# Kernel optimization log

Hardware: AMD Instinct MI355X
Metric: run time of the kernel (lower is better)

## Reference

```python
import jax, jax.numpy as jnp
import numpy as np

ROI = 9
GROUPS = 32

def _gn(x, gamma, beta, eps):
    B, C, H, W = x.shape
    xr = x.reshape(B, GROUPS, C // GROUPS, H, W)
    m = xr.mean(axis=(2, 3, 4), keepdims=True)
    v = xr.var(axis=(2, 3, 4), keepdims=True)
    xr = (xr - m) / jnp.sqrt(v + eps)
    x = xr.reshape(B, C, H, W)
    if gamma is not None:
        x = x * gamma[None, :, None, None] + beta[None, :, None, None]
    return x

def _conv(x, w, b, pad):
    y = jax.lax.conv_general_dilated(x, w, (1, 1), [(pad, pad), (pad, pad)],
                                     dimension_numbers=('NCHW', 'OIHW', 'NCHW'))
    return y + b[None, :, None, None]

def _roi_align(feat, boxes):
    # torchvision roi_align, spatial_scale=1, aligned=False (roi size clamped to >=1),
    # adaptive sampling ratio -> 1 sample/bin for sub-pixel normalized boxes.
    B, C, H, W = feat.shape
    x1, y1, x2, y2 = boxes[:, 0], boxes[:, 1], boxes[:, 2], boxes[:, 3]
    rw = jnp.maximum(x2 - x1, 1.0)
    rh = jnp.maximum(y2 - y1, 1.0)
    ctr = (jnp.arange(ROI, dtype=feat.dtype) + 0.5) / ROI
    xs = x1[:, None] + ctr[None, :] * rw[:, None]  # [B,ROI]
    ys = y1[:, None] + ctr[None, :] * rh[:, None]
    def samp(img, ysr, xsr):
        yc = jnp.clip(ysr, 0.0, H - 1.0)
        xc = jnp.clip(xsr, 0.0, W - 1.0)
        y0 = jnp.floor(yc).astype(jnp.int32)
        x0 = jnp.floor(xc).astype(jnp.int32)
        y1i = jnp.minimum(y0 + 1, H - 1)
        x1i = jnp.minimum(x0 + 1, W - 1)
        ly = yc - y0
        lx = xc - x0
        v00 = img[:, y0[:, None], x0[None, :]]
        v01 = img[:, y0[:, None], x1i[None, :]]
        v10 = img[:, y1i[:, None], x0[None, :]]
        v11 = img[:, y1i[:, None], x1i[None, :]]
        w00 = (1 - ly)[:, None] * (1 - lx)[None, :]
        w01 = (1 - ly)[:, None] * lx[None, :]
        w10 = ly[:, None] * (1 - lx)[None, :]
        w11 = ly[:, None] * lx[None, :]
        return v00 * w00 + v01 * w01 + v10 * w10 + v11 * w11
    return jax.vmap(samp)(feat, ys, xs)

def _paste(global_x, x_local, bbox):
    # per-box nearest interpolate of 9x9 patch to (y2-y1, x2-x1) and additive scatter,
    # expressed as a dense gather over the full HxW grid (jit-friendly).
    B, C, H, W = global_x.shape
    bb = jnp.floor(bbox * H).astype(jnp.int32)  # bbox >= 0 so trunc == floor
    x1b, y1b = bb[:, 0], bb[:, 1]
    x2b = jnp.maximum(bb[:, 2], x1b + 1)
    y2b = jnp.maximum(bb[:, 3], y1b + 1)
    r = jnp.arange(H)
    jy = r[None, :] - y1b[:, None]
    jx = r[None, :] - x1b[:, None]
    oh = (y2b - y1b)[:, None]
    ow = (x2b - x1b)[:, None]
    sy = jnp.clip((jy * ROI) // oh, 0, ROI - 1)  # F.interpolate 'nearest': floor(j*in/out)
    sx = jnp.clip((jx * ROI) // ow, 0, ROI - 1)
    iny = (jy >= 0) & (r[None, :] < y2b[:, None])
    inx = (jx >= 0) & (r[None, :] < x2b[:, None])
    m = iny[:, :, None] & inx[:, None, :]  # [B,H,W]
    def one(xi, syi, sxi, mi):
        return jnp.where(mi[None], xi[:, syi][:, :, sxi], 0.0)
    return global_x + jax.vmap(one)(x_local, sy, sx, m)

def reference(global_x, context, indicator, bbox, cond_flag,
              ln_g, ln_b, cn_g, cn_b, Wq, bq, Wk, bk, Wv, bv, Wsg, bsg, Wsb, bsb):
    B, C, H, W = global_x.shape
    T, D = context.shape[1], context.shape[2]
    Hc = 16
    ctx_map = jnp.transpose(context, (0, 2, 1)).reshape(B, D, Hc, Hc)
    ctx_mean = jnp.mean(context, axis=1, keepdims=True)              # [B,1,D]
    mean_map = jnp.transpose(ctx_mean, (0, 2, 1))[:, :, :, None]     # [B,D,1,1]
    ctx_map = jnp.where(cond_flag[:, None, None, None], ctx_map, mean_map)
    ctx = jnp.where(cond_flag[:, None, None], context, ctx_mean)
    x = _roi_align(global_x, bbox)                                   # [B,C,9,9]
    x = _gn(x, ln_g, ln_b, 1e-6)
    ind = jnp.broadcast_to(indicator[:, :, None, None], (B, indicator.shape[1], ROI, ROI))
    x = jnp.concatenate([x, ind], axis=1)
    q = _conv(x, Wq, bq, 0).reshape(B, C, ROI * ROI).transpose(0, 2, 1)        # [B,81,C]
    k = _conv(_gn(ctx_map, cn_g, cn_b, 1e-6), Wk, bk, 0).reshape(B, C, T).transpose(0, 2, 1)
    v = _conv(ctx_map, Wv, bv, 1).reshape(B, C, T).transpose(0, 2, 1)
    attn = jax.nn.softmax(jnp.einsum('bic,bjc->bij', q, k), axis=-1)  # no scale (as in source)
    xa = jnp.einsum('bij,bjc->bic', attn, v).transpose(0, 2, 1).reshape(B, C, ROI, ROI)
    ac = jnp.einsum('bij,bjd->bid', attn, ctx).transpose(0, 2, 1).reshape(B, D, ROI, ROI)
    x = _gn(xa, None, None, 1e-5) * _conv(ac, Wsg, bsg, 1) + _conv(ac, Wsb, bsb, 1)  # SPADE
    out = _paste(global_x, x, bbox)
    return (out, attn)

def setup_inputs():
    key = jax.random.key(0)
    ks = jax.random.split(key, 12)
    B, C, H, D, T = 32, 320, 64, 1024, 256
    s = 0.02
    global_x = jax.random.normal(ks[0], (B, C, H, H), jnp.float32)
    context = jax.random.normal(ks[1], (B, T, D), jnp.float32)
    indicator = (jax.random.uniform(ks[2], (B, 2)) > 0.5).astype(jnp.float32)
    c0 = jax.random.uniform(ks[3], (B, 2), minval=0.05, maxval=0.5)
    wh = jax.random.uniform(ks[4], (B, 2), minval=0.15, maxval=0.45)
    bbox = jnp.concatenate([c0, jnp.minimum(c0 + wh, 1.0)], axis=1)
    cond_flag = jax.random.randint(ks[5], (B,), 0, 2) > 0
    return {
        'global_x': global_x, 'context': context, 'indicator': indicator,
        'bbox': bbox, 'cond_flag': cond_flag,
        'ln_g': jnp.ones((C,)), 'ln_b': jnp.zeros((C,)),
        'cn_g': jnp.ones((D,)), 'cn_b': jnp.zeros((D,)),
        'Wq': jax.random.normal(ks[6], (C, C + 2, 1, 1)) * s, 'bq': jnp.zeros((C,)),
        'Wk': jax.random.normal(ks[7], (C, D, 1, 1)) * s, 'bk': jnp.zeros((C,)),
        'Wv': jax.random.normal(ks[8], (C, D, 3, 3)) * s, 'bv': jnp.zeros((C,)),
        'Wsg': jax.random.normal(ks[9], (C, D, 3, 3)) * s, 'bsg': jnp.zeros((C,)),
        'Wsb': jax.random.normal(ks[10], (C, D, 3, 3)) * s, 'bsb': jnp.zeros((C,)),
    }
```

## Files before the change

kernel.cpp:

```cpp
#include <hip/hip_runtime.h>
#include <hip/hip_bf16.h>

#define DINLINE __device__ __forceinline__

typedef short short8 __attribute__((ext_vector_type(8)));
typedef float f32x4 __attribute__((ext_vector_type(4)));
typedef unsigned short u16;

DINLINE u16 f2b(float f) {
  __hip_bfloat16 h = __float2bfloat16(f);
  return *reinterpret_cast<u16*>(&h);
}
DINLINE float b2f(u16 u) {
  __hip_bfloat16 h = *reinterpret_cast<__hip_bfloat16*>(&u);
  return __bfloat162float(h);
}

DINLINE void gload16(const u16* g, u16* l) {
  __builtin_amdgcn_global_load_lds((const __attribute__((address_space(1))) void*)g,
                                   (__attribute__((address_space(3))) void*)l, 16, 0, 0);
}

DINLINE void wave_red2(float& s, float& s2) {
  for (int o = 32; o > 0; o >>= 1) { s += __shfl_down(s, o); s2 += __shfl_down(s2, o); }
}

__global__ void k_prep0(const float* __restrict__ ctx, const int* __restrict__ cond,
                        const float* __restrict__ gx, const float* __restrict__ bbox,
                        const float* __restrict__ Wk, const float* __restrict__ Wq,
                        const float* __restrict__ Wv, const float* __restrict__ Wsg,
                        const float* __restrict__ Wsb,
                        float* __restrict__ cmean, float* __restrict__ stats,
                        float* __restrict__ roix, u16* __restrict__ oK, u16* __restrict__ oQ,
                        u16* __restrict__ Wv_r, u16* __restrict__ Wsgsb) {
  __shared__ float shf[4][2];
  __shared__ float cp[8][32];
  __shared__ float cm32[32];
  __shared__ int iy0[9], iy1[9], ix0[9], ix1[9];
  __shared__ float fly[9], flx[9];
  __shared__ u16 l[9216];
  int bid = blockIdx.x;
  int tid = threadIdx.x;

  if (bid < 1024) {
    int b = bid >> 5, g = bid & 31;
    const float* src = ctx + (size_t)b * 262144 + g * 32;
    int c = tid & 31, tg = tid >> 5;
    float cs = 0.f, s = 0.f, s2 = 0.f;
#pragma unroll 4
    for (int k = 0; k < 32; ++k) {
      int t = tg + k * 8;
      float v = src[(size_t)t * 1024 + c];
      cs += v; s += v; s2 += v * v;
    }
    cp[tg][c] = cs;
    wave_red2(s, s2);
    int lane = tid & 63, w = tid >> 6;
    if (lane == 0) { shf[w][0] = s; shf[w][1] = s2; }
    __syncthreads();
    if (tid < 32) {
      float colsum = 0.f;
#pragma unroll
      for (int k = 0; k < 8; ++k) colsum += cp[k][tid];
      float mv = colsum * (1.f / 256.f);
      cmean[b * 1024 + g * 32 + tid] = mv;
      cm32[tid] = mv;
    }
    __syncthreads();
    if (tid == 0) {
      float m, var;
      if (cond[b]) {
        float ts = shf[0][0] + shf[1][0] + shf[2][0] + shf[3][0];
        float ts2 = shf[0][1] + shf[1][1] + shf[2][1] + shf[3][1];
        m = ts * (1.f / 8192.f);
        var = ts2 * (1.f / 8192.f) - m * m;
      } else {
        float ms = 0.f, ms2 = 0.f;
#pragma unroll
        for (int k = 0; k < 32; ++k) { ms += cm32[k]; ms2 += cm32[k] * cm32[k]; }
        m = ms * (1.f / 32.f);
        var = ms2 * (1.f / 32.f) - m * m;
      }
      stats[bid * 2] = m;
      stats[bid * 2 + 1] = 1.f / sqrtf(var + 1e-6f);
    }
    return;
  }
  if (bid < 1056) {
    int b = bid - 1024;
    int t = tid;
    if (t < 9) {
      float x1 = bbox[b * 4 + 0], y1 = bbox[b * 4 + 1], x2 = bbox[b * 4 + 2], y2 = bbox[b * 4 + 3];
      float rw = fmaxf(x2 - x1, 1.f), rh = fmaxf(y2 - y1, 1.f);
      float ctr = ((float)t + 0.5f) / 9.0f;
      float yc = fminf(fmaxf(y1 + ctr * rh, 0.f), 63.f);
      int y0 = (int)floorf(yc);
      iy0[t] = y0; iy1[t] = min(y0 + 1, 63); fly[t] = yc - (float)y0;
      float xc = fminf(fmaxf(x1 + ctr * rw, 0.f), 63.f);
      int x0 = (int)floorf(xc);
      ix0[t] = x0; ix1[t] = min(x0 + 1, 63); flx[t] = xc - (float)x0;
    }
    __syncthreads();
    for (int idx = t; idx < 320 * 81; idx += 256) {
      int c = idx / 81, p = idx - c * 81;
      int py = p / 9, px = p - py * 9;
      const float* img = gx + ((size_t)b * 320 + c) * 4096;
      float ly = fly[py], lx = flx[px];
      float v00 = img[iy0[py] * 64 + ix0[px]];
      float v01 = img[iy0[py] * 64 + ix1[px]];
      float v10 = img[iy1[py] * 64 + ix0[px]];
      float v11 = img[iy1[py] * 64 + ix1[px]];
      roix[((size_t)b * 320 + c) * 81 + p] =
          v00 * (1.f - ly) * (1.f - lx) + v01 * (1.f - ly) * lx + v10 * ly * (1.f - lx) + v11 * ly * lx;
    }
    return;
  }
  int bid2 = bid - 1056;
  if (bid2 < 1536) {
    int i = bid2 * 256 + tid;
    int c = i >> 10, d = i & 1023;
    float v = (i < 327680) ? Wk[i] : 0.f;
    u16 hi = f2b(v), lo = f2b(v - b2f(hi));
    u16* p = oK + (size_t)c * 2048 + d;
    p[0] = hi; p[1024] = lo;
    return;
  }
  if (bid2 < 2016) {
    int i = (bid2 - 1536) * 256 + tid;
    if (i >= 122880) return;
    int c = i / 384, k = i - c * 384;
    float v = (k < 322) ? Wq[c * 322 + k] : 0.f;
    u16 hi = f2b(v), lo = f2b(v - b2f(hi));
    u16* p = oQ + (size_t)c * 768 + k;
    p[0] = hi; p[384] = lo;
    return;
  }
  int cc = bid2 - 2016;
  const float* src = nullptr; u16* dst;
  if (cc < 384) { dst = Wv_r + (size_t)cc * 9216; if (cc < 320) src = Wv + (size_t)cc * 9216; }
  else if (cc < 704) { src = Wsg + (size_t)(cc - 384) * 9216; dst = Wsgsb + (size_t)(cc - 384) * 9216; }
  else { src = Wsb + (size_t)(cc - 704) * 9216; dst = Wsgsb + (size_t)(320 + cc - 704) * 9216; }
  if (src == nullptr) {
    for (int i = tid; i < 9216; i += 256) dst[i] = 0;
    return;
  }
  for (int i = tid; i < 9216; i += 256) l[i] = f2b(src[i]);
  __syncthreads();
  for (int i = tid; i < 9216; i += 256) {
    int r = i >> 10, d = i & 1023;
    dst[i] = l[d * 9 + r];
  }
}

__global__ void k_ctx_prep(const float* __restrict__ ctx, const float* __restrict__ cmean,
                           const float* __restrict__ st, const float* __restrict__ cng,
                           const float* __restrict__ cnb, const int* __restrict__ cond,
                           u16* __restrict__ sel, u16* __restrict__ bvc, u16* __restrict__ cn2) {
  __shared__ u16 tile[64][66];
  int b = blockIdx.z;
  int t0 = blockIdx.x * 64;
  int d0 = blockIdx.y * 64;
  bool cf = cond[b] != 0;
#pragma unroll
  for (int q = 0; q < 16; ++q) {
    int idx = q * 256 + threadIdx.x;
    int r = idx >> 6, c = idx & 63;
    int t = t0 + r, d = d0 + c;
    float v = cf ? ctx[((size_t)b * 256 + t) * 1024 + d] : cmean[b * 1024 + d];
    u16 sv = f2b(v);
    sel[((size_t)b * 256 + t) * 1024 + d] = sv;
    tile[r][c] = sv;
    int gi = (b << 5) + (d >> 5);
    float nv = (v - st[gi * 2]) * st[gi * 2 + 1] * cng[d] + cnb[d];
    u16 hi = f2b(nv);
    u16 lo = f2b(nv - b2f(hi));
    size_t rbase = ((size_t)b * 256 + t) * 2048;
    cn2[rbase + d] = hi;
    cn2[rbase + 1024 + d] = lo;
  }
  __syncthreads();
#pragma unroll
  for (int q = 0; q < 16; ++q) {
    int idx = q * 256 + threadIdx.x;
    int r = idx >> 6, c = idx & 63;
    bvc[((size_t)b * 1344 + 320 + d0 + r) * 256 + t0 + c] = tile[c][r];
  }
}

__global__ void k_stats810(const float* __restrict__ src, float* __restrict__ stats, float eps) {
  int bg = blockIdx.x;
  const float* p = src + (size_t)bg * 810;
  float s = 0.f, s2 = 0.f;
  for (int i = threadIdx.x; i < 810; i += 256) { float v = p[i]; s += v; s2 += v * v; }
  wave_red2(s, s2);
  __shared__ float sh[4][2];
  int lane = threadIdx.x & 63, w = threadIdx.x >> 6;
  if (lane == 0) { sh[w][0] = s; sh[w][1] = s2; }
  __syncthreads();
  if (threadIdx.x == 0) {
    s = sh[0][0] + sh[1][0] + sh[2][0] + sh[3][0];
    s2 = sh[0][1] + sh[1][1] + sh[2][1] + sh[3][1];
    float m = s * (1.f / 810.f);
    float var = s2 * (1.f / 810.f) - m * m;
    stats[bg * 2] = m;
    stats[bg * 2 + 1] = 1.f / sqrtf(var + eps);
  }
}

__global__ void k_stats_xa(const float* __restrict__ xa, float* __restrict__ stats) {
  int bg = blockIdx.x; int b = bg >> 5, g = bg & 31;
  float s = 0.f, s2 = 0.f;
  for (int e = threadIdx.x; e < 810; e += 256) {
    int i = e / 10, cc = e - i * 10;
    float v = xa[((long)b * 128 + i) * 320 + g * 10 + cc];
    s += v; s2 += v * v;
  }
  wave_red2(s, s2);
  __shared__ float sh[4][2];
  int lane = threadIdx.x & 63, w = threadIdx.x >> 6;
  if (lane == 0) { sh[w][0] = s; sh[w][1] = s2; }
  __syncthreads();
  if (threadIdx.x == 0) {
    s = sh[0][0] + sh[1][0] + sh[2][0] + sh[3][0];
    s2 = sh[0][1] + sh[1][1] + sh[2][1] + sh[3][1];
    float m = s * (1.f / 810.f);
    float var = s2 * (1.f / 810.f) - m * m;
    stats[bg * 2] = m;
    stats[bg * 2 + 1] = 1.f / sqrtf(var + 1e-5f);
  }
}

__global__ void k_aq2(const float* __restrict__ roix, const float* __restrict__ st,
                      const float* __restrict__ lng, const float* __restrict__ lnb,
                      const float* __restrict__ ind, u16* __restrict__ o) {
  int i = blockIdx.x * 256 + threadIdx.x;
  if (i >= 32 * 128 * 384) return;
  int b = i / (128 * 384), rem = i - b * (128 * 384);
  int row = rem / 384, k = rem - row * 384;
  float v = 0.f;
  if (row < 81) {
    if (k < 320) {
      float x = roix[((size_t)b * 320 + k) * 81 + row];
      int gi = (b << 5) + k / 10;
      v = (x - st[gi * 2]) * st[gi * 2 + 1] * lng[k] + lnb[k];
    } else if (k < 322) v = ind[b * 2 + (k - 320)];
  }
  u16 hi = f2b(v);
  u16 lo = f2b(v - b2f(hi));
  u16* p = o + ((size_t)b * 128 + row) * 768 + k;
  p[0] = hi; p[384] = lo;
}

__global__ void k_sumv_t(const float* __restrict__ buf, long pstride,
                         const float* __restrict__ bv, u16* __restrict__ bvc) {
  __shared__ u16 tile[64][66];
  int b = blockIdx.z, t0 = blockIdx.x * 64, j0 = blockIdx.y * 64;
#pragma unroll
  for (int q = 0; q < 16; ++q) {
    int idx = q * 256 + threadIdx.x;
    int r = idx >> 6, c = idx & 63;
    long p = (long)b * 256 + t0 + r;
    const float* src = buf + p * 384 + j0 + c;
    float v = src[0] + src[pstride] + src[2 * pstride] + bv[j0 + c];
    tile[r][c] = f2b(v);
  }
  __syncthreads();
#pragma unroll
  for (int q = 0; q < 16; ++q) {
    int idx = q * 256 + threadIdx.x;
    int r = idx >> 6, c = idx & 63;
    bvc[((long)b * 1344 + j0 + r) * 256 + t0 + c] = tile[c][r];
  }
}

__global__ void k_softmax2(float* __restrict__ attn, u16* __restrict__ attn_bf) {
  int i = blockIdx.x, b = blockIdx.y;
  int t = threadIdx.x;
  if (i >= 81) { attn_bf[((size_t)b * 128 + i) * 256 + t] = 0; return; }
  float* p = attn + ((size_t)b * 81 + i) * 256;
  float v = p[t];
  float m = v;
  for (int o = 32; o > 0; o >>= 1) m = fmaxf(m, __shfl_down(m, o));
  __shared__ float sm[4], ss[4];
  if ((t & 63) == 0) sm[t >> 6] = m;
  __syncthreads();
  m = fmaxf(fmaxf(sm[0], sm[1]), fmaxf(sm[2], sm[3]));
  float e = expf(v - m);
  float s = e;
  for (int o = 32; o > 0; o >>= 1) s += __shfl_down(s, o);
  if ((t & 63) == 0) ss[t >> 6] = s;
  __syncthreads();
  s = ss[0] + ss[1] + ss[2] + ss[3];
  float r = e / s;
  p[t] = r;
  attn_bf[((size_t)b * 128 + i) * 256 + t] = f2b(r);
}

__global__ void k_paste(const float* __restrict__ gx, const float* __restrict__ bbox,
                        const float* __restrict__ xl, float* __restrict__ out) {
  int bc = blockIdx.x;
  int b = bc / 320;
  int c = bc - b * 320;
  __shared__ int sy[64], sx[64];
  __shared__ unsigned char my[64], mx[64];
  int x1b = (int)floorf(bbox[b * 4 + 0] * 64.f);
  int y1b = (int)floorf(bbox[b * 4 + 1] * 64.f);
  int x2b = max((int)floorf(bbox[b * 4 + 2] * 64.f), x1b + 1);
  int y2b = max((int)floorf(bbox[b * 4 + 3] * 64.f), y1b + 1);
  int t = threadIdx.x;
  if (t < 64) {
    int jy = t - y1b, oh = y2b - y1b;
    my[t] = (jy >= 0 && t < y2b) ? 1 : 0;
    sy[t] = my[t] ? min(jy * 9 / oh, 8) : 0;
    int jx = t - x1b, ow = x2b - x1b;
    mx[t] = (jx >= 0 && t < x2b) ? 1 : 0;
    sx[t] = mx[t] ? min(jx * 9 / ow, 8) : 0;
  }
  __syncthreads();
  size_t base = (size_t)bc * 4096;
  const float* xlb = xl + ((long)b * 81) * 320 + c;
  const float4* g4 = (const float4*)(gx + base);
  float4* o4 = (float4*)(out + base);
#pragma unroll
  for (int it = 0; it < 4; ++it) {
    int idx = it * 256 + t;
    int y = idx >> 4, x0 = (idx & 15) << 2;
    float4 v = g4[idx];
    if (my[y]) {
      const float* row = xlb + (long)sy[y] * 9 * 320;
      if (mx[x0 + 0]) v.x += row[(long)sx[x0 + 0] * 320];
      if (mx[x0 + 1]) v.y += row[(long)sx[x0 + 1] * 320];
      if (mx[x0 + 2]) v.z += row[(long)sx[x0 + 2] * 320];
      if (mx[x0 + 3]) v.w += row[(long)sx[x0 + 3] * 320];
    }
    o4[idx] = v;
  }
}


struct RowA {
  const u16* A; int physW;
  struct RS { const u16* base; };
  DINLINE RS row(long p) const { return { A + p * (long)physW }; }
  DINLINE const u16* ptr(const RS& rs, int kk) const { return rs.base + (kk << 6); }
};
struct TriA {
  const u16* A; int physW; int nhi;
  struct RS { const u16* base; };
  DINLINE RS row(long p) const { return { A + p * (long)physW }; }
  DINLINE const u16* ptr(const RS& rs, int kk) const {
    int c = (int)(((unsigned)kk * 171u) >> 9), r = kk - 3 * c;
    return rs.base + (((r == 1 ? nhi : 0) + c) << 6);
  }
};
struct ShiftVA {
  const u16* src; const u16* zp;
  struct RS { int y, x; const u16* bbase; };
  DINLINE RS row(long p) const {
    int b = (int)(p >> 8), ps = (int)p & 255;
    return { ps >> 4, ps & 15, src + ((long)b << 18) };
  }
  DINLINE const u16* ptr(const RS& rs, int kk) const {
    int c = (int)(((unsigned)kk * 57u) >> 9), s = kk - 9 * c;
    int sy = (s * 11) >> 5, sx = s - sy * 3;
    int yy = rs.y + sy - 1, xx = rs.x + sx - 1;
    bool ok = ((unsigned)yy < 16u) & ((unsigned)xx < 16u);
    return ok ? rs.bbase + (((yy << 4) + xx) << 10) + (c << 6) : zp;
  }
};
struct Shift9A {
  const u16* src; const u16* zp;
  struct RS { int y, x; const u16* bbase; int pin; };
  DINLINE RS row(long p) const {
    int pi = (int)p;
    int b = pi / 81, pp = pi - b * 81;
    int pin = pi < 2592 ? 1 : 0;
    if (b > 31) b = 31;
    return { pp / 9, pp % 9, src + ((long)b << 17), pin };
  }
  DINLINE const u16* ptr(const RS& rs, int kk) const {
    int c = (int)(((unsigned)kk * 57u) >> 9), s = kk - 9 * c;
    int sy = (s * 11) >> 5, sx = s - sy * 3;
    int yy = rs.y + sy - 1, xx = rs.x + sx - 1;
    bool ok = rs.pin && ((unsigned)yy < 9u) && ((unsigned)xx < 9u);
    return ok ? rs.bbase + ((yy * 9 + xx) << 10) + (c << 6) : zp;
  }
};


struct RowB {
  const u16* B; int physW; long bstride;
  struct RS { const u16* base; };
  DINLINE RS row(int by, long j) const { return { B + ((long)(by >> 1) * bstride + j) * physW }; }
  DINLINE const u16* ptr(const RS& rs, int kk) const { return rs.base + (kk << 6); }
};
struct TriB {
  const u16* B; int physW; int nhi; long bstride;
  struct RS { const u16* base; };
  DINLINE RS row(int by, long j) const { return { B + ((long)(by >> 1) * bstride + j) * physW }; }
  DINLINE const u16* ptr(const RS& rs, int kk) const {
    int c = (int)(((unsigned)kk * 171u) >> 9), r = kk - 3 * c;
    return rs.base + (((r == 2 ? nhi : 0) + c) << 6);
  }
};
struct ShiftWB {
  const u16* W;
  struct RS { const u16* base; };
  DINLINE RS row(int, long j) const { return { W + j * 9216 }; }
  DINLINE const u16* ptr(const RS& rs, int kk) const {
    int c = (int)(((unsigned)kk * 57u) >> 9), s = kk - 9 * c;
    return rs.base + (s << 10) + (c << 6);
  }
};


struct EpiHiLo {
  u16* o; const float* bias;
  DINLINE void operator()(long p, int j, float v) const {
    v += bias[j];
    u16 hi = f2b(v), lo = f2b(v - b2f(hi));
    u16* q = o + p * 640 + j;
    q[0] = hi; q[320] = lo;
  }
};
struct EpiLog {
  float* attn;
  DINLINE void operator()(long p, int j, float v) const {
    int b = (int)(p >> 7), i = (int)p & 127;
    if (i < 81) attn[((long)b * 81 + i) * 256 + j] = v;
  }
};
struct EpiXaAc {
  float* xa; u16* ac;
  DINLINE void operator()(long p, int j, float v) const {
    int b = (int)(p >> 7), i = (int)p & 127;
    if (j < 320) {
      xa[((long)b * 128 + i) * 320 + j] = v;
    } else {
      ac[((long)b * 128 + i) * 1024 + (j - 320)] = f2b(v);
    }
  }
};
struct EpiPart {
  float* buf; long pstride; int jw;
  DINLINE void operator()(int part, long p, int j, float v) const {
    buf[(long)part * pstride + p * (long)jw + j] = v;
  }
};


template <class AS, class BS, class EPI>
__global__ __launch_bounds__(256, 4) void gemm_pipe(AS a, BS bsrc, int gy, int nch, EPI epi) {
  __shared__ u16 As[2][4096];
  __shared__ u16 Bs[2][4096];
  const int N = gridDim.x;
  const int q = N >> 3, r8 = N & 7;
  const int j8 = blockIdx.x & 7, pos = blockIdx.x >> 3;
  const int lid = (j8 < r8) ? j8 * (q + 1) + pos : r8 * (q + 1) + (j8 - r8) * q + pos;
  const int by = lid % gy, bx = lid / gy;

  const int tid = threadIdx.x;
  const int w = tid >> 6, lane = tid & 63;
  const int wm = w >> 1, wn = w & 1;
  const long p0 = (long)by * 64;
  const int j0 = bx * 64;

  const int r0 = tid >> 3;
  const int csw = (((lane & 7) ^ (lane >> 3)) << 3);
  auto rsA0 = a.row(p0 + r0);
  auto rsA1 = a.row(p0 + r0 + 32);
  auto rsB0 = bsrc.row(by, j0 + r0);
  auto rsB1 = bsrc.row(by, j0 + r0 + 32);
  u16* lA0 = (u16*)As + w * 512;
  u16* lA1 = (u16*)As + 2048 + w * 512;
  u16* lB0 = (u16*)Bs + w * 512;
  u16* lB1 = (u16*)Bs + 2048 + w * 512;

  f32x4 acc[2][2];
#pragma unroll
  for (int x = 0; x < 2; ++x)
#pragma unroll
    for (int y = 0; y < 2; ++y) acc[x][y] = (f32x4){0.f, 0.f, 0.f, 0.f};

  const int fr = lane & 15, fs = lane >> 4, fx = lane & 7;
  const int arow0 = (wm * 32 + fr) * 64;
  const int brow0 = (wn * 32 + fr) * 64;

  gload16(a.ptr(rsA0, 0) + csw, lA0);
  gload16(a.ptr(rsA1, 0) + csw, lA1);
  gload16(bsrc.ptr(rsB0, 0) + csw, lB0);
  gload16(bsrc.ptr(rsB1, 0) + csw, lB1);

  for (int kk = 0; kk < nch; ++kk) {
    const int cur = kk & 1;
    if (kk + 1 < nch) {
      const int nxt = cur ^ 1;
      gload16(a.ptr(rsA0, kk + 1) + csw, lA0 + nxt * 4096);
      gload16(a.ptr(rsA1, kk + 1) + csw, lA1 + nxt * 4096);
      gload16(bsrc.ptr(rsB0, kk + 1) + csw, lB0 + nxt * 4096);
      gload16(bsrc.ptr(rsB1, kk + 1) + csw, lB1 + nxt * 4096);
      asm volatile("s_waitcnt vmcnt(4)" ::: "memory");
    } else {
      asm volatile("s_waitcnt vmcnt(0)" ::: "memory");
    }
    __builtin_amdgcn_s_barrier();
    __builtin_amdgcn_sched_barrier(0);
    short8 af[2][2], bf[2][2];
#pragma unroll
    for (int fm = 0; fm < 2; ++fm)
#pragma unroll
      for (int kh = 0; kh < 2; ++kh) {
        int slot = ((((kh << 2) | fs) ^ fx) << 3);
        af[fm][kh] = *(const short8*)(&As[cur][arow0 + fm * 1024 + slot]);
      }
#pragma unroll
    for (int fn = 0; fn < 2; ++fn)
#pragma unroll
      for (int kh = 0; kh < 2; ++kh) {
        int slot = ((((kh << 2) | fs) ^ fx) << 3);
        bf[fn][kh] = *(const short8*)(&Bs[cur][brow0 + fn * 1024 + slot]);
      }
#pragma unroll
    for (int kh = 0; kh < 2; ++kh)
#pragma unroll
      for (int fm = 0; fm < 2; ++fm)
#pragma unroll
        for (int fn = 0; fn < 2; ++fn)
          acc[fm][fn] = __builtin_amdgcn_mfma_f32_16x16x32_bf16(af[fm][kh], bf[fn][kh], acc[fm][fn], 0, 0, 0);
    __builtin_amdgcn_sched_barrier(0);
    __builtin_amdgcn_s_barrier();
  }

  const long ip = p0 + wm * 32 + fs * 4;
  const int jb = j0 + wn * 32 + fr;
#pragma unroll
  for (int fm = 0; fm < 2; ++fm)
#pragma unroll
    for (int fn = 0; fn < 2; ++fn)
#pragma unroll
      for (int rr = 0; rr < 4; ++rr)
        epi(ip + fm * 16 + rr, jb + fn * 16, acc[fm][fn][rr]);
}


template <class AS, class BS, class EPI>
__global__ __launch_bounds__(256, 3) void gemm128(AS a, BS bsrc, int gy, int gp, int nchw, EPI epi) {
  __shared__ u16 As[8192];
  __shared__ u16 Bs[8192];
  const int N = gridDim.x;
  const int q = N >> 3, r8 = N & 7;
  const int j8 = blockIdx.x & 7, pos = blockIdx.x >> 3;
  const int lid = (j8 < r8) ? j8 * (q + 1) + pos : r8 * (q + 1) + (j8 - r8) * q + pos;
  const int gyp = gy * gp;
  const int bx = lid / gyp;
  const int rem = lid - bx * gyp;
  const int by = rem % gy;
  const int part = rem / gy;
  const int k0 = part * nchw;

  const int tid = threadIdx.x;
  const int w = tid >> 6, lane = tid & 63;
  const int wm = w >> 1, wn = w & 1;
  const long p0 = (long)by * 128;
  const int j0 = bx * 128;

  const int r0 = tid >> 3;
  const int csw = (((lane & 7) ^ (lane >> 3)) << 3);
  typename AS::RS rsA[4];
  typename BS::RS rsB[4];
#pragma unroll
  for (int i = 0; i < 4; ++i) {
    rsA[i] = a.row(p0 + r0 + 32 * i);
    rsB[i] = bsrc.row(by, (long)j0 + r0 + 32 * i);
  }

  f32x4 acc[4][4];
#pragma unroll
  for (int x = 0; x < 4; ++x)
#pragma unroll
    for (int y = 0; y < 4; ++y) acc[x][y] = (f32x4){0.f, 0.f, 0.f, 0.f};

  const int fr = lane & 15, fs = lane >> 4, fx = lane & 7;

  for (int kk = 0; kk < nchw; ++kk) {
    __syncthreads();
#pragma unroll
    for (int i = 0; i < 4; ++i) {
      gload16(a.ptr(rsA[i], k0 + kk) + csw, As + (i * 32 + w * 8) * 64);
      gload16(bsrc.ptr(rsB[i], k0 + kk) + csw, Bs + (i * 32 + w * 8) * 64);
    }
    __syncthreads();
#pragma unroll
    for (int kh = 0; kh < 2; ++kh) {
      const int slot = ((((kh << 2) | fs) ^ fx) << 3);
      short8 af[4], bf[4];
#pragma unroll
      for (int i = 0; i < 4; ++i) {
        af[i] = *(const short8*)(As + (wm * 64 + i * 16 + fr) * 64 + slot);
        bf[i] = *(const short8*)(Bs + (wn * 64 + i * 16 + fr) * 64 + slot);
      }
#pragma unroll
      for (int fm = 0; fm < 4; ++fm)
#pragma unroll
        for (int fn = 0; fn < 4; ++fn)
          acc[fm][fn] = __builtin_amdgcn_mfma_f32_16x16x32_bf16(af[fm], bf[fn], acc[fm][fn], 0, 0, 0);
    }
  }

  const long ip = p0 + wm * 64 + fs * 4;
  const int jb = j0 + wn * 64 + fr;
#pragma unroll
  for (int fm = 0; fm < 4; ++fm)
#pragma unroll
    for (int fn = 0; fn < 4; ++fn)
#pragma unroll
      for (int rr = 0; rr < 4; ++rr)
        epi(part, ip + fm * 16 + rr, jb + fn * 16, acc[fm][fn][rr]);
}

template <class EPI>
__global__ void k_sum_parts(const float* __restrict__ buf, long pstride, int np,
                            int jw, int jvalid, EPI epi) {
  long p = blockIdx.x;
  const float* src = buf + p * (long)jw;
  for (int j = threadIdx.x; j < jvalid; j += 256) {
    float v = 0.f;
    for (int t = 0; t < np; ++t) v += src[t * pstride + j];
    epi(p, j, v);
  }
}

__global__ void k_sum_sgsb(const float* __restrict__ buf, long pstride,
                           const float* __restrict__ bsg, const float* __restrict__ bsb,
                           const float* __restrict__ xa, const float* __restrict__ st,
                           float* __restrict__ xl) {
  __shared__ float sgb[640];
  __shared__ float ms[32], rss[32];
  long p = blockIdx.x;
  int b = (int)(p / 81), pp = (int)(p - (long)b * 81);
  const float* src = buf + p * 640;
  for (int j = threadIdx.x; j < 640; j += 256) {
    float v = 0.f;
#pragma unroll
    for (int t = 0; t < 4; ++t) v += src[t * pstride + j];
    sgb[j] = v + (j < 320 ? bsg[j] : bsb[j - 320]);
  }
  if (threadIdx.x < 32) {
    ms[threadIdx.x] = st[(b * 32 + threadIdx.x) * 2];
    rss[threadIdx.x] = st[(b * 32 + threadIdx.x) * 2 + 1];
  }
  __syncthreads();
  for (int c = threadIdx.x; c < 320; c += 256) {
    int g = c / 10;
    float xv = xa[((long)b * 128 + pp) * 320 + c];
    xl[((long)b * 81 + pp) * 320 + c] = (xv - ms[g]) * rss[g] * sgb[c] + sgb[320 + c];
  }
}


extern "C" void kernel_launch(void* const* d_in, const int* in_sizes, int n_in,
                              void* d_out, int out_size, void* d_ws, size_t ws_size,
                              hipStream_t stream) {
  const float* gx   = (const float*)d_in[0];
  const float* ctx  = (const float*)d_in[1];
  const float* ind  = (const float*)d_in[2];
  const float* bbox = (const float*)d_in[3];
  const int*   cond = (const int*)d_in[4];
  const float* ln_g = (const float*)d_in[5];
  const float* ln_b = (const float*)d_in[6];
  const float* cn_g = (const float*)d_in[7];
  const float* cn_b = (const float*)d_in[8];
  const float* Wq = (const float*)d_in[9];   const float* bq = (const float*)d_in[10];
  const float* Wk = (const float*)d_in[11];  const float* bk = (const float*)d_in[12];
  const float* Wv = (const float*)d_in[13];  const float* bv = (const float*)d_in[14];
  const float* Wsg = (const float*)d_in[15]; const float* bsg = (const float*)d_in[16];
  const float* Wsb = (const float*)d_in[17]; const float* bsb = (const float*)d_in[18];

  char* base = (char*)d_out;
  float* out = (float*)d_out;
  float* attn_out = out + (size_t)41943040;

  u16* sel     = (u16*)(base + 0);
  u16* bvc     = (u16*)(base + 16777216);
  u16* cn2     = (u16*)(base + 38797312);
  u16* Aq2     = (u16*)(base + 72351744);
  float* part_f= (float*)(base + 38797312);
  u16* k2      = (u16*)(base + 78643200);
  u16* q2      = (u16*)(base + 89128960);
  u16* attn_bf = (u16*)(base + 94371840);
  u16* ac_bf   = (u16*)(base + 96468992);
  u16* Wk2     = (u16*)(base + 108175360);
  u16* Wq2     = (u16*)(base + 109748224);
  u16* Wv_r    = (u16*)(base + 110239744);
  u16* Wsgsb   = (u16*)(base + 117317632);
  float* partK = (float*)(base + 129114112);
  float* xa_f  = (float*)(base + 154279936);
  u16* zpage   = Wv_r + (size_t)320 * 9216;

  float* cmean = (float*)d_ws;
  float* cnst  = cmean + 32768;
  float* lnst  = cnst + 2048;
  float* xast  = lnst + 2048;
  float* roix  = xast + 2048;
  float* xloc  = roix + 829440;

  k_prep0<<<4096, 256, 0, stream>>>(ctx, cond, gx, bbox, Wk, Wq, Wv, Wsg, Wsb,
                                    cmean, cnst, roix, Wk2, Wq2, Wv_r, Wsgsb);
  k_ctx_prep<<<dim3(4, 16, 32), 256, 0, stream>>>(ctx, cmean, cnst, cn_g, cn_b, cond, sel, bvc, cn2);
  k_stats810<<<1024, 256, 0, stream>>>(roix, lnst, 1e-6f);
  k_aq2<<<6144, 256, 0, stream>>>(roix, lnst, ln_g, ln_b, ind, Aq2);

  gemm128<<<384, 256, 0, stream>>>(TriA{cn2, 2048, 16}, TriB{Wk2, 2048, 16, 0},
                                   64, 2, 24, EpiPart{partK, (long)8192 * 384, 384});
  k_sum_parts<<<8192, 256, 0, stream>>>(partK, (long)8192 * 384, 2, 384, 320, EpiHiLo{k2, bk});
  gemm_pipe<<<320, 256, 0, stream>>>(TriA{Aq2, 768, 6}, TriB{Wq2, 768, 6, 0},
                                     64, 18, EpiHiLo{q2, bq});
  gemm128<<<576, 256, 0, stream>>>(ShiftVA{sel, zpage}, ShiftWB{Wv_r},
                                   64, 3, 48, EpiPart{part_f, (long)8192 * 384, 384});
  k_sumv_t<<<dim3(4, 5, 32), 256, 0, stream>>>(part_f, (long)8192 * 384, bv, bvc);
  gemm_pipe<<<256, 256, 0, stream>>>(TriA{q2, 640, 5}, TriB{k2, 640, 5, 256},
                                     64, 15, EpiLog{attn_out});
  k_softmax2<<<dim3(128, 32), 256, 0, stream>>>(attn_out, attn_bf);
  gemm_pipe<<<1344, 256, 0, stream>>>(RowA{attn_bf, 256}, RowB{bvc, 256, 1344},
                                      64, 4, EpiXaAc{xa_f, ac_bf});
  k_stats_xa<<<1024, 256, 0, stream>>>(xa_f, xast);
  gemm128<<<420, 256, 0, stream>>>(Shift9A{ac_bf, zpage}, ShiftWB{Wsgsb},
                                   21, 4, 36, EpiPart{part_f, (long)2688 * 640, 640});
  k_sum_sgsb<<<2592, 256, 0, stream>>>(part_f, (long)2688 * 640, bsg, bsb, xa_f, xast, xloc);

  k_paste<<<10240, 256, 0, stream>>>(gx, bbox, xloc, out);
}
```

Before: 350.9 us.

## Merge independent kernels into combined launches and rebalance split-K GEMMs

Several independent stages are packed into single launches that branch on block index: context prep with LN stats, the K/V/Q GEMMs, the V-sum transpose with the QK GEMM, and the xa stats with the conv GEMM. The K GEMM drops split-K and writes its hi/lo bf16 output directly, removing a separate partial-sum kernel. The V GEMM goes from three K-splits to two. The aim is fewer launches and less partial-buffer traffic, with independent work running concurrently. The cost is heterogeneous blocks sharing one register and LDS budget, plus longer per-block K loops.

```diff
diff --git a/kernel.cpp b/kernel.cpp
--- a/kernel.cpp
+++ b/kernel.cpp
@@ -23,6 +23,293 @@
 
 DINLINE void wave_red2(float& s, float& s2) {
   for (int o = 32; o > 0; o >>= 1) { s += __shfl_down(s, o); s2 += __shfl_down(s2, o); }
+}
+
+
+struct RowA {
+  const u16* A; int physW;
+  struct RS { const u16* base; };
+  DINLINE RS row(long p) const { return { A + p * (long)physW }; }
+  DINLINE const u16* ptr(const RS& rs, int kk) const { return rs.base + (kk << 6); }
+};
+struct TriA {
+  const u16* A; int physW; int nhi;
+  struct RS { const u16* base; };
+  DINLINE RS row(long p) const { return { A + p * (long)physW }; }
+  DINLINE const u16* ptr(const RS& rs, int kk) const {
+    int c = (int)(((unsigned)kk * 171u) >> 9), r = kk - 3 * c;
+    return rs.base + (((r == 1 ? nhi : 0) + c) << 6);
+  }
+};
+struct ShiftVA {
+  const u16* src; const u16* zp;
+  struct RS { int y, x; const u16* bbase; };
+  DINLINE RS row(long p) const {
+    int b = (int)(p >> 8), ps = (int)p & 255;
+    return { ps >> 4, ps & 15, src + ((long)b << 18) };
+  }
+  DINLINE const u16* ptr(const RS& rs, int kk) const {
+    int c = (int)(((unsigned)kk * 57u) >> 9), s = kk - 9 * c;
+    int sy = (s * 11) >> 5, sx = s - sy * 3;
+    int yy = rs.y + sy - 1, xx = rs.x + sx - 1;
+    bool ok = ((unsigned)yy < 16u) & ((unsigned)xx < 16u);
+    return ok ? rs.bbase + (((yy << 4) + xx) << 10) + (c << 6) : zp;
+  }
+};
+struct Shift9A {
+  const u16* src; const u16* zp;
+  struct RS { int y, x; const u16* bbase; int pin; };
+  DINLINE RS row(long p) const {
+    int pi = (int)p;
+    int b = pi / 81, pp = pi - b * 81;
+    int pin = pi < 2592 ? 1 : 0;
+    if (b > 31) b = 31;
+    return { pp / 9, pp % 9, src + ((long)b << 17), pin };
+  }
+  DINLINE const u16* ptr(const RS& rs, int kk) const {
+    int c = (int)(((unsigned)kk * 57u) >> 9), s = kk - 9 * c;
+    int sy = (s * 11) >> 5, sx = s - sy * 3;
+    int yy = rs.y + sy - 1, xx = rs.x + sx - 1;
+    bool ok = rs.pin && ((unsigned)yy < 9u) && ((unsigned)xx < 9u);
+    return ok ? rs.bbase + ((yy * 9 + xx) << 10) + (c << 6) : zp;
+  }
+};
+
+
+struct RowB {
+  const u16* B; int physW; long bstride;
+  struct RS { const u16* base; };
+  DINLINE RS row(int by, long j) const { return { B + ((long)(by >> 1) * bstride + j) * physW }; }
+  DINLINE const u16* ptr(const RS& rs, int kk) const { return rs.base + (kk << 6); }
+};
+struct TriB {
+  const u16* B; int physW; int nhi; long bstride;
+  struct RS { const u16* base; };
+  DINLINE RS row(int by, long j) const { return { B + ((long)(by >> 1) * bstride + j) * physW }; }
+  DINLINE const u16* ptr(const RS& rs, int kk) const {
+    int c = (int)(((unsigned)kk * 171u) >> 9), r = kk - 3 * c;
+    return rs.base + (((r == 2 ? nhi : 0) + c) << 6);
+  }
+};
+struct ShiftWB {
+  const u16* W;
+  struct RS { const u16* base; };
+  DINLINE RS row(int, long j) const { return { W + j * 9216 }; }
+  DINLINE const u16* ptr(const RS& rs, int kk) const {
+    int c = (int)(((unsigned)kk * 57u) >> 9), s = kk - 9 * c;
+    return rs.base + (s << 10) + (c << 6);
+  }
+};
+
+
+struct EpiHiLo {
+  u16* o; const float* bias;
+  DINLINE void operator()(long p, int j, float v) const {
+    v += bias[j];
+    u16 hi = f2b(v), lo = f2b(v - b2f(hi));
+    u16* q = o + p * 640 + j;
+    q[0] = hi; q[320] = lo;
+  }
+};
+struct EpiHiLoP {
+  u16* o; const float* bias;
+  DINLINE void operator()(int, long p, int j, float v) const {
+    if (j >= 320) return;
+    v += bias[j];
+    u16 hi = f2b(v), lo = f2b(v - b2f(hi));
+    u16* q = o + p * 640 + j;
+    q[0] = hi; q[320] = lo;
+  }
+};
+struct EpiLog {
+  float* attn;
+  DINLINE void operator()(long p, int j, float v) const {
+    int b = (int)(p >> 7), i = (int)p & 127;
+    if (i < 81) attn[((long)b * 81 + i) * 256 + j] = v;
+  }
+};
+struct EpiXaAc {
+  float* xa; u16* ac;
+  DINLINE void operator()(long p, int j, float v) const {
+    int b = (int)(p >> 7), i = (int)p & 127;
+    if (j < 320) {
+      xa[((long)b * 128 + i) * 320 + j] = v;
+    } else {
+      ac[((long)b * 128 + i) * 1024 + (j - 320)] = f2b(v);
+    }
+  }
+};
+struct EpiPart {
+  float* buf; long pstride; int jw;
+  DINLINE void operator()(int part, long p, int j, float v) const {
+    buf[(long)part * pstride + p * (long)jw + j] = v;
+  }
+};
+
+
+template <class AS, class BS, class EPI>
+DINLINE void gemm_pipe_body(u16* lds, AS a, BS bsrc, int gy, int nch, EPI epi,
+                            int subN, int bid) {
+  const int q = subN >> 3, r8 = subN & 7;
+  const int j8 = bid & 7, pos = bid >> 3;
+  const int lid = (j8 < r8) ? j8 * (q + 1) + pos : r8 * (q + 1) + (j8 - r8) * q + pos;
+  const int by = lid % gy, bx = lid / gy;
+
+  const int tid = threadIdx.x;
+  const int w = tid >> 6, lane = tid & 63;
+  const int wm = w >> 1, wn = w & 1;
+  const long p0 = (long)by * 64;
+  const int j0 = bx * 64;
+
+  const int r0 = tid >> 3;
+  const int csw = (((lane & 7) ^ (lane >> 3)) << 3);
+  auto rsA0 = a.row(p0 + r0);
+  auto rsA1 = a.row(p0 + r0 + 32);
+  auto rsB0 = bsrc.row(by, j0 + r0);
+  auto rsB1 = bsrc.row(by, j0 + r0 + 32);
+  u16* lA0 = lds + w * 512;
+  u16* lA1 = lds + 2048 + w * 512;
+  u16* lB0 = lds + 8192 + w * 512;
+  u16* lB1 = lds + 8192 + 2048 + w * 512;
+
+  f32x4 acc[2][2];
+#pragma unroll
+  for (int x = 0; x < 2; ++x)
+#pragma unroll
+    for (int y = 0; y < 2; ++y) acc[x][y] = (f32x4){0.f, 0.f, 0.f, 0.f};
+
+  const int fr = lane & 15, fs = lane >> 4, fx = lane & 7;
+  const int arow0 = (wm * 32 + fr) * 64;
+  const int brow0 = (wn * 32 + fr) * 64;
+
+  gload16(a.ptr(rsA0, 0) + csw, lA0);
+  gload16(a.ptr(rsA1, 0) + csw, lA1);
+  gload16(bsrc.ptr(rsB0, 0) + csw, lB0);
+  gload16(bsrc.ptr(rsB1, 0) + csw, lB1);
+
+  for (int kk = 0; kk < nch; ++kk) {
+    const int cur = kk & 1;
+    if (kk + 1 < nch) {
+      const int nxt = cur ^ 1;
+      gload16(a.ptr(rsA0, kk + 1) + csw, lA0 + nxt * 4096);
+      gload16(a.ptr(rsA1, kk + 1) + csw, lA1 + nxt * 4096);
+      gload16(bsrc.ptr(rsB0, kk + 1) + csw, lB0 + nxt * 4096);
+      gload16(bsrc.ptr(rsB1, kk + 1) + csw, lB1 + nxt * 4096);
+      asm volatile("s_waitcnt vmcnt(4)" ::: "memory");
+    } else {
+      asm volatile("s_waitcnt vmcnt(0)" ::: "memory");
+    }
+    __builtin_amdgcn_s_barrier();
+    __builtin_amdgcn_sched_barrier(0);
+    short8 af[2][2], bf[2][2];
+#pragma unroll
+    for (int fm = 0; fm < 2; ++fm)
+#pragma unroll
+      for (int kh = 0; kh < 2; ++kh) {
+        int slot = ((((kh << 2) | fs) ^ fx) << 3);
+        af[fm][kh] = *(const short8*)(lds + cur * 4096 + arow0 + fm * 1024 + slot);
+      }
+#pragma unroll
+    for (int fn = 0; fn < 2; ++fn)
+#pragma unroll
+      for (int kh = 0; kh < 2; ++kh) {
+        int slot = ((((kh << 2) | fs) ^ fx) << 3);
+        bf[fn][kh] = *(const short8*)(lds + 8192 + cur * 4096 + brow0 + fn * 1024 + slot);
+      }
+#pragma unroll
+    for (int kh = 0; kh < 2; ++kh)
+#pragma unroll
+      for (int fm = 0; fm < 2; ++fm)
+#pragma unroll
+        for (int fn = 0; fn < 2; ++fn)
+          acc[fm][fn] = __builtin_amdgcn_mfma_f32_16x16x32_bf16(af[fm][kh], bf[fn][kh], acc[fm][fn], 0, 0, 0);
+    __builtin_amdgcn_sched_barrier(0);
+    __builtin_amdgcn_s_barrier();
+  }
+
+  const long ip = p0 + wm * 32 + fs * 4;
+  const int jb = j0 + wn * 32 + fr;
+#pragma unroll
+  for (int fm = 0; fm < 2; ++fm)
+#pragma unroll
+    for (int fn = 0; fn < 2; ++fn)
+#pragma unroll
+      for (int rr = 0; rr < 4; ++rr)
+        epi(ip + fm * 16 + rr, jb + fn * 16, acc[fm][fn][rr]);
+}
+
+
+template <class AS, class BS, class EPI>
+DINLINE void gemm128_body(u16* lds, AS a, BS bsrc, int gy, int gp, int nchw, EPI epi,
+                          int subN, int bid) {
+  const int q = subN >> 3, r8 = subN & 7;
+  const int j8 = bid & 7, pos = bid >> 3;
+  const int lid = (j8 < r8) ? j8 * (q + 1) + pos : r8 * (q + 1) + (j8 - r8) * q + pos;
+  const int gyp = gy * gp;
+  const int bx = lid / gyp;
+  const int rem = lid - bx * gyp;
+  const int by = rem % gy;
+  const int part = rem / gy;
+  const int k0 = part * nchw;
+
+  const int tid = threadIdx.x;
+  const int w = tid >> 6, lane = tid & 63;
+  const int wm = w >> 1, wn = w & 1;
+  const long p0 = (long)by * 128;
+  const int j0 = bx * 128;
+
+  const int r0 = tid >> 3;
+  const int csw = (((lane & 7) ^ (lane >> 3)) << 3);
+  typename AS::RS rsA[4];
+  typename BS::RS rsB[4];
+#pragma unroll
+  for (int i = 0; i < 4; ++i) {
+    rsA[i] = a.row(p0 + r0 + 32 * i);
+    rsB[i] = bsrc.row(by, (long)j0 + r0 + 32 * i);
+  }
+
+  f32x4 acc[4][4];
+#pragma unroll
+  for (int x = 0; x < 4; ++x)
+#pragma unroll
+    for (int y = 0; y < 4; ++y) acc[x][y] = (f32x4){0.f, 0.f, 0.f, 0.f};
+
+  const int fr = lane & 15, fs = lane >> 4, fx = lane & 7;
+
+  for (int kk = 0; kk < nchw; ++kk) {
+    __syncthreads();
+#pragma unroll
+    for (int i = 0; i < 4; ++i) {
+      gload16(a.ptr(rsA[i], k0 + kk) + csw, lds + (i * 32 + w * 8) * 64);
+      gload16(bsrc.ptr(rsB[i], k0 + kk) + csw, lds + 8192 + (i * 32 + w * 8) * 64);
+    }
+    __syncthreads();
+#pragma unroll
+    for (int kh = 0; kh < 2; ++kh) {
+      const int slot = ((((kh << 2) | fs) ^ fx) << 3);
+      short8 af[4], bf[4];
+#pragma unroll
+      for (int i = 0; i < 4; ++i) {
+        af[i] = *(const short8*)(lds + (wm * 64 + i * 16 + fr) * 64 + slot);
+        bf[i] = *(const short8*)(lds + 8192 + (wn * 64 + i * 16 + fr) * 64 + slot);
+      }
+#pragma unroll
+      for (int fm = 0; fm < 4; ++fm)
+#pragma unroll
+        for (int fn = 0; fn < 4; ++fn)
+          acc[fm][fn] = __builtin_amdgcn_mfma_f32_16x16x32_bf16(af[fm], bf[fn], acc[fm][fn], 0, 0, 0);
+    }
+  }
+
+  const long ip = p0 + wm * 64 + fs * 4;
+  const int jb = j0 + wn * 64 + fr;
+#pragma unroll
+  for (int fm = 0; fm < 4; ++fm)
+#pragma unroll
+    for (int fn = 0; fn < 4; ++fn)
+#pragma unroll
+      for (int rr = 0; rr < 4; ++rr)
+        epi(part, ip + fm * 16 + rr, jb + fn * 16, acc[fm][fn][rr]);
 }
 
 __global__ void k_prep0(const float* __restrict__ ctx, const int* __restrict__ cond,
@@ -152,48 +439,51 @@
   }
 }
 
-__global__ void k_ctx_prep(const float* __restrict__ ctx, const float* __restrict__ cmean,
-                           const float* __restrict__ st, const float* __restrict__ cng,
-                           const float* __restrict__ cnb, const int* __restrict__ cond,
-                           u16* __restrict__ sel, u16* __restrict__ bvc, u16* __restrict__ cn2) {
+__global__ __launch_bounds__(256) void k_prep1(
+    const float* __restrict__ ctx, const float* __restrict__ cmean,
+    const float* __restrict__ st, const float* __restrict__ cng,
+    const float* __restrict__ cnb, const int* __restrict__ cond,
+    u16* __restrict__ sel, u16* __restrict__ bvc, u16* __restrict__ cn2,
+    const float* __restrict__ roix, float* __restrict__ lnst) {
   __shared__ u16 tile[64][66];
-  int b = blockIdx.z;
-  int t0 = blockIdx.x * 64;
-  int d0 = blockIdx.y * 64;
-  bool cf = cond[b] != 0;
-#pragma unroll
-  for (int q = 0; q < 16; ++q) {
-    int idx = q * 256 + threadIdx.x;
-    int r = idx >> 6, c = idx & 63;
-    int t = t0 + r, d = d0 + c;
-    float v = cf ? ctx[((size_t)b * 256 + t) * 1024 + d] : cmean[b * 1024 + d];
-    u16 sv = f2b(v);
-    sel[((size_t)b * 256 + t) * 1024 + d] = sv;
-    tile[r][c] = sv;
-    int gi = (b << 5) + (d >> 5);
-    float nv = (v - st[gi * 2]) * st[gi * 2 + 1] * cng[d] + cnb[d];
-    u16 hi = f2b(nv);
-    u16 lo = f2b(nv - b2f(hi));
-    size_t rbase = ((size_t)b * 256 + t) * 2048;
-    cn2[rbase + d] = hi;
-    cn2[rbase + 1024 + d] = lo;
-  }
-  __syncthreads();
-#pragma unroll
-  for (int q = 0; q < 16; ++q) {
-    int idx = q * 256 + threadIdx.x;
-    int r = idx >> 6, c = idx & 63;
-    bvc[((size_t)b * 1344 + 320 + d0 + r) * 256 + t0 + c] = tile[c][r];
-  }
-}
-
-__global__ void k_stats810(const float* __restrict__ src, float* __restrict__ stats, float eps) {
-  int bg = blockIdx.x;
-  const float* p = src + (size_t)bg * 810;
+  __shared__ float sh[4][2];
+  int bid = blockIdx.x;
+  if (bid < 2048) {
+    int b = bid >> 6;
+    int d0 = ((bid >> 2) & 15) * 64;
+    int t0 = (bid & 3) * 64;
+    bool cf = cond[b] != 0;
+#pragma unroll
+    for (int q = 0; q < 16; ++q) {
+      int idx = q * 256 + threadIdx.x;
+      int r = idx >> 6, c = idx & 63;
+      int t = t0 + r, d = d0 + c;
+      float v = cf ? ctx[((size_t)b * 256 + t) * 1024 + d] : cmean[b * 1024 + d];
+      u16 sv = f2b(v);
+      sel[((size_t)b * 256 + t) * 1024 + d] = sv;
+      tile[r][c] = sv;
+      int gi = (b << 5) + (d >> 5);
+      float nv = (v - st[gi * 2]) * st[gi * 2 + 1] * cng[d] + cnb[d];
+      u16 hi = f2b(nv);
+      u16 lo = f2b(nv - b2f(hi));
+      size_t rbase = ((size_t)b * 256 + t) * 2048;
+      cn2[rbase + d] = hi;
+      cn2[rbase + 1024 + d] = lo;
+    }
+    __syncthreads();
+#pragma unroll
+    for (int q = 0; q < 16; ++q) {
+      int idx = q * 256 + threadIdx.x;
+      int r = idx >> 6, c = idx & 63;
+      bvc[((size_t)b * 1344 + 320 + d0 + r) * 256 + t0 + c] = tile[c][r];
+    }
+    return;
+  }
+  int bg = bid - 2048;
+  const float* p = roix + (size_t)bg * 810;
   float s = 0.f, s2 = 0.f;
   for (int i = threadIdx.x; i < 810; i += 256) { float v = p[i]; s += v; s2 += v * v; }
   wave_red2(s, s2);
-  __shared__ float sh[4][2];
   int lane = threadIdx.x & 63, w = threadIdx.x >> 6;
   if (lane == 0) { sh[w][0] = s; sh[w][1] = s2; }
   __syncthreads();
@@ -202,31 +492,8 @@
     s2 = sh[0][1] + sh[1][1] + sh[2][1] + sh[3][1];
     float m = s * (1.f / 810.f);
     float var = s2 * (1.f / 810.f) - m * m;
-    stats[bg * 2] = m;
-    stats[bg * 2 + 1] = 1.f / sqrtf(var + eps);
-  }
-}
-
-__global__ void k_stats_xa(const float* __restrict__ xa, float* __restrict__ stats) {
-  int bg = blockIdx.x; int b = bg >> 5, g = bg & 31;
-  float s = 0.f, s2 = 0.f;
-  for (int e = threadIdx.x; e < 810; e += 256) {
-    int i = e / 10, cc = e - i * 10;
-    float v = xa[((long)b * 128 + i) * 320 + g * 10 + cc];
-    s += v; s2 += v * v;
-  }
-  wave_red2(s, s2);
-  __shared__ float sh[4][2];
-  int lane = threadIdx.x & 63, w = threadIdx.x >> 6;
-  if (lane == 0) { sh[w][0] = s; sh[w][1] = s2; }
-  __syncthreads();
-  if (threadIdx.x == 0) {
-    s = sh[0][0] + sh[1][0] + sh[2][0] + sh[3][0];
-    s2 = sh[0][1] + sh[1][1] + sh[2][1] + sh[3][1];
-    float m = s * (1.f / 810.f);
-    float var = s2 * (1.f / 810.f) - m * m;
-    stats[bg * 2] = m;
-    stats[bg * 2 + 1] = 1.f / sqrtf(var + 1e-5f);
+    lnst[bg * 2] = m;
+    lnst[bg * 2 + 1] = 1.f / sqrtf(var + 1e-6f);
   }
 }
 
@@ -251,26 +518,56 @@
   p[0] = hi; p[384] = lo;
 }
 
-__global__ void k_sumv_t(const float* __restrict__ buf, long pstride,
-                         const float* __restrict__ bv, u16* __restrict__ bvc) {
-  __shared__ u16 tile[64][66];
-  int b = blockIdx.z, t0 = blockIdx.x * 64, j0 = blockIdx.y * 64;
-#pragma unroll
-  for (int q = 0; q < 16; ++q) {
-    int idx = q * 256 + threadIdx.x;
-    int r = idx >> 6, c = idx & 63;
-    long p = (long)b * 256 + t0 + r;
-    const float* src = buf + p * 384 + j0 + c;
-    float v = src[0] + src[pstride] + src[2 * pstride] + bv[j0 + c];
-    tile[r][c] = f2b(v);
-  }
-  __syncthreads();
-#pragma unroll
-  for (int q = 0; q < 16; ++q) {
-    int idx = q * 256 + threadIdx.x;
-    int r = idx >> 6, c = idx & 63;
-    bvc[((long)b * 1344 + j0 + r) * 256 + t0 + c] = tile[c][r];
-  }
+__global__ __launch_bounds__(256, 3) void k_gemms(
+    const u16* __restrict__ cn2, const u16* __restrict__ Wk2, u16* __restrict__ k2,
+    const float* __restrict__ bk,
+    const u16* __restrict__ sel, const u16* __restrict__ Wv_r, const u16* __restrict__ zpage,
+    float* __restrict__ partV,
+    const u16* __restrict__ Aq2, const u16* __restrict__ Wq2, u16* __restrict__ q2,
+    const float* __restrict__ bq) {
+  __shared__ u16 lds[16384];
+  int bid = blockIdx.x;
+  if (bid < 192) {
+    gemm128_body(lds, TriA{cn2, 2048, 16}, TriB{Wk2, 2048, 16, 0}, 64, 1, 48,
+                 EpiHiLoP{k2, bk}, 192, bid);
+  } else if (bid < 576) {
+    gemm128_body(lds, ShiftVA{sel, zpage}, ShiftWB{Wv_r}, 64, 2, 72,
+                 EpiPart{partV, (long)8192 * 384, 384}, 384, bid - 192);
+  } else {
+    gemm_pipe_body(lds, TriA{Aq2, 768, 6}, TriB{Wq2, 768, 6, 0}, 64, 18,
+                   EpiHiLo{q2, bq}, 320, bid - 576);
+  }
+}
+
+__global__ __launch_bounds__(256, 4) void k_mid(
+    const float* __restrict__ partV, const float* __restrict__ bv, u16* __restrict__ bvc,
+    const u16* __restrict__ q2, const u16* __restrict__ k2, float* __restrict__ attn) {
+  __shared__ u16 lds[16384];
+  int bid = blockIdx.x;
+  if (bid < 640) {
+    int b = bid / 20, rem = bid - b * 20;
+    int t0 = (rem & 3) * 64, j0 = (rem >> 2) * 64;
+    const long pstride = (long)8192 * 384;
+#pragma unroll
+    for (int q = 0; q < 16; ++q) {
+      int idx = q * 256 + threadIdx.x;
+      int r = idx >> 6, c = idx & 63;
+      long p = (long)b * 256 + t0 + r;
+      const float* src = partV + p * 384 + j0 + c;
+      float v = src[0] + src[pstride] + bv[j0 + c];
+      lds[r * 66 + c] = f2b(v);
+    }
+    __syncthreads();
+#pragma unroll
+    for (int q = 0; q < 16; ++q) {
+      int idx = q * 256 + threadIdx.x;
+      int r = idx >> 6, c = idx & 63;
+      bvc[((long)b * 1344 + j0 + r) * 256 + t0 + c] = lds[c * 66 + r];
+    }
+    return;
+  }
+  gemm_pipe_body(lds, TriA{q2, 640, 5}, TriB{k2, 640, 5, 256}, 64, 15,
+                 EpiLog{attn}, 256, bid - 640);
 }
 
 __global__ void k_softmax2(float* __restrict__ attn, u16* __restrict__ attn_bf) {
@@ -296,6 +593,72 @@
   attn_bf[((size_t)b * 128 + i) * 256 + t] = f2b(r);
 }
 
+template <class AS, class BS, class EPI>
+__global__ __launch_bounds__(256, 4) void gemm_pipe(AS a, BS bsrc, int gy, int nch, EPI epi) {
+  __shared__ u16 lds[16384];
+  gemm_pipe_body(lds, a, bsrc, gy, nch, epi, gridDim.x, blockIdx.x);
+}
+
+__global__ __launch_bounds__(256, 3) void k_post(
+    const float* __restrict__ xa, float* __restrict__ xast,
+    const u16* __restrict__ ac_bf, const u16* __restrict__ zpage,
+    const u16* __restrict__ Wsgsb, float* __restrict__ part_f) {
+  __shared__ u16 lds[16384];
+  int bid = blockIdx.x;
+  if (bid < 1024) {
+    int b = bid >> 5, g = bid & 31;
+    float s = 0.f, s2 = 0.f;
+    for (int e = threadIdx.x; e < 810; e += 256) {
+      int i = e / 10, cc = e - i * 10;
+      float v = xa[((long)b * 128 + i) * 320 + g * 10 + cc];
+      s += v; s2 += v * v;
+    }
+    wave_red2(s, s2);
+    float* sh = (float*)lds;
+    int lane = threadIdx.x & 63, w = threadIdx.x >> 6;
+    if (lane == 0) { sh[w * 2] = s; sh[w * 2 + 1] = s2; }
+    __syncthreads();
+    if (threadIdx.x == 0) {
+      s = sh[0] + sh[2] + sh[4] + sh[6];
+      s2 = sh[1] + sh[3] + sh[5] + sh[7];
+      float m = s * (1.f / 810.f);
+      float var = s2 * (1.f / 810.f) - m * m;
+      xast[bid * 2] = m;
+      xast[bid * 2 + 1] = 1.f / sqrtf(var + 1e-5f);
+    }
+    return;
+  }
+  gemm128_body(lds, Shift9A{ac_bf, zpage}, ShiftWB{Wsgsb}, 21, 4, 36,
+               EpiPart{part_f, (long)2688 * 640, 640}, 420, bid - 1024);
+}
+
+__global__ void k_sum_sgsb(const float* __restrict__ buf, long pstride,
+                           const float* __restrict__ bsg, const float* __restrict__ bsb,
+                           const float* __restrict__ xa, const float* __restrict__ st,
+                           float* __restrict__ xl) {
+  __shared__ float sgb[640];
+  __shared__ float ms[32], rss[32];
+  long p = blockIdx.x;
+  int b = (int)(p / 81), pp = (int)(p - (long)b * 81);
+  const float* src = buf + p * 640;
+  for (int j = threadIdx.x; j < 640; j += 256) {
+    float v = 0.f;
+#pragma unroll
+    for (int t = 0; t < 4; ++t) v += src[t * pstride + j];
+    sgb[j] = v + (j < 320 ? bsg[j] : bsb[j - 320]);
+  }
+  if (threadIdx.x < 32) {
+    ms[threadIdx.x] = st[(b * 32 + threadIdx.x) * 2];
+    rss[threadIdx.x] = st[(b * 32 + threadIdx.x) * 2 + 1];
+  }
+  __syncthreads();
+  for (int c = threadIdx.x; c < 320; c += 256) {
+    int g = c / 10;
+    float xv = xa[((long)b * 128 + pp) * 320 + c];
+    xl[((long)b * 81 + pp) * 320 + c] = (xv - ms[g]) * rss[g] * sgb[c] + sgb[320 + c];
+  }
+}
+
 __global__ void k_paste(const float* __restrict__ gx, const float* __restrict__ bbox,
                         const float* __restrict__ xl, float* __restrict__ out) {
   int bc = blockIdx.x;
@@ -338,326 +701,6 @@
 }
 
 
-struct RowA {
-  const u16* A; int physW;
-  struct RS { const u16* base; };
-  DINLINE RS row(long p) const { return { A + p * (long)physW }; }
-  DINLINE const u16* ptr(const RS& rs, int kk) const { return rs.base + (kk << 6); }
-};
-struct TriA {
-  const u16* A; int physW; int nhi;
-  struct RS { const u16* base; };
-  DINLINE RS row(long p) const { return { A + p * (long)physW }; }
-  DINLINE const u16* ptr(const RS& rs, int kk) const {
-    int c = (int)(((unsigned)kk * 171u) >> 9), r = kk - 3 * c;
-    return rs.base + (((r == 1 ? nhi : 0) + c) << 6);
-  }
-};
-struct ShiftVA {
-  const u16* src; const u16* zp;
-  struct RS { int y, x; const u16* bbase; };
-  DINLINE RS row(long p) const {
-    int b = (int)(p >> 8), ps = (int)p & 255;
-    return { ps >> 4, ps & 15, src + ((long)b << 18) };
-  }
-  DINLINE const u16* ptr(const RS& rs, int kk) const {
-    int c = (int)(((unsigned)kk * 57u) >> 9), s = kk - 9 * c;
-    int sy = (s * 11) >> 5, sx = s - sy * 3;
-    int yy = rs.y + sy - 1, xx = rs.x + sx - 1;
-    bool ok = ((unsigned)yy < 16u) & ((unsigned)xx < 16u);
-    return ok ? rs.bbase + (((yy << 4) + xx) << 10) + (c << 6) : zp;
-  }
-};
-struct Shift9A {
-  const u16* src; const u16* zp;
-  struct RS { int y, x; const u16* bbase; int pin; };
-  DINLINE RS row(long p) const {
-    int pi = (int)p;
-    int b = pi / 81, pp = pi - b * 81;
-    int pin = pi < 2592 ? 1 : 0;
-    if (b > 31) b = 31;
-    return { pp / 9, pp % 9, src + ((long)b << 17), pin };
-  }
-  DINLINE const u16* ptr(const RS& rs, int kk) const {
-    int c = (int)(((unsigned)kk * 57u) >> 9), s = kk - 9 * c;
-    int sy = (s * 11) >> 5, sx = s - sy * 3;
-    int yy = rs.y + sy - 1, xx = rs.x + sx - 1;
-    bool ok = rs.pin && ((unsigned)yy < 9u) && ((unsigned)xx < 9u);
-    return ok ? rs.bbase + ((yy * 9 + xx) << 10) + (c << 6) : zp;
-  }
-};
-
-
-struct RowB {
-  const u16* B; int physW; long bstride;
-  struct RS { const u16* base; };
-  DINLINE RS row(int by, long j) const { return { B + ((long)(by >> 1) * bstride + j) * physW }; }
-  DINLINE const u16* ptr(const RS& rs, int kk) const { return rs.base + (kk << 6); }
-};
-struct TriB {
-  const u16* B; int physW; int nhi; long bstride;
-  struct RS { const u16* base; };
-  DINLINE RS row(int by, long j) const { return { B + ((long)(by >> 1) * bstride + j) * physW }; }
-  DINLINE const u16* ptr(const RS& rs, int kk) const {
-    int c = (int)(((unsigned)kk * 171u) >> 9), r = kk - 3 * c;
-    return rs.base + (((r == 2 ? nhi : 0) + c) << 6);
-  }
-};
-struct ShiftWB {
-  const u16* W;
-  struct RS { const u16* base; };
-  DINLINE RS row(int, long j) const { return { W + j * 9216 }; }
-  DINLINE const u16* ptr(const RS& rs, int kk) const {
-    int c = (int)(((unsigned)kk * 57u) >> 9), s = kk - 9 * c;
-    return rs.base + (s << 10) + (c << 6);
-  }
-};
-
-
-struct EpiHiLo {
-  u16* o; const float* bias;
-  DINLINE void operator()(long p, int j, float v) const {
-    v += bias[j];
-    u16 hi = f2b(v), lo = f2b(v - b2f(hi));
-    u16* q = o + p * 640 + j;
-    q[0] = hi; q[320] = lo;
-  }
-};
-struct EpiLog {
-  float* attn;
-  DINLINE void operator()(long p, int j, float v) const {
-    int b = (int)(p >> 7), i = (int)p & 127;
-    if (i < 81) attn[((long)b * 81 + i) * 256 + j] = v;
-  }
-};
-struct EpiXaAc {
-  float* xa; u16* ac;
-  DINLINE void operator()(long p, int j, float v) const {
-    int b = (int)(p >> 7), i = (int)p & 127;
-    if (j < 320) {
-      xa[((long)b * 128 + i) * 320 + j] = v;
-    } else {
-      ac[((long)b * 128 + i) * 1024 + (j - 320)] = f2b(v);
-    }
-  }
-};
-struct EpiPart {
-  float* buf; long pstride; int jw;
-  DINLINE void operator()(int part, long p, int j, float v) const {
-    buf[(long)part * pstride + p * (long)jw + j] = v;
-  }
-};
-
-
-template <class AS, class BS, class EPI>
-__global__ __launch_bounds__(256, 4) void gemm_pipe(AS a, BS bsrc, int gy, int nch, EPI epi) {
-  __shared__ u16 As[2][4096];
-  __shared__ u16 Bs[2][4096];
-  const int N = gridDim.x;
-  const int q = N >> 3, r8 = N & 7;
-  const int j8 = blockIdx.x & 7, pos = blockIdx.x >> 3;
-  const int lid = (j8 < r8) ? j8 * (q + 1) + pos : r8 * (q + 1) + (j8 - r8) * q + pos;
-  const int by = lid % gy, bx = lid / gy;
-
-  const int tid = threadIdx.x;
-  const int w = tid >> 6, lane = tid & 63;
-  const int wm = w >> 1, wn = w & 1;
-  const long p0 = (long)by * 64;
-  const int j0 = bx * 64;
-
-  const int r0 = tid >> 3;
-  const int csw = (((lane & 7) ^ (lane >> 3)) << 3);
-  auto rsA0 = a.row(p0 + r0);
-  auto rsA1 = a.row(p0 + r0 + 32);
-  auto rsB0 = bsrc.row(by, j0 + r0);
-  auto rsB1 = bsrc.row(by, j0 + r0 + 32);
-  u16* lA0 = (u16*)As + w * 512;
-  u16* lA1 = (u16*)As + 2048 + w * 512;
-  u16* lB0 = (u16*)Bs + w * 512;
-  u16* lB1 = (u16*)Bs + 2048 + w * 512;
-
-  f32x4 acc[2][2];
-#pragma unroll
-  for (int x = 0; x < 2; ++x)
-#pragma unroll
-    for (int y = 0; y < 2; ++y) acc[x][y] = (f32x4){0.f, 0.f, 0.f, 0.f};
-
-  const int fr = lane & 15, fs = lane >> 4, fx = lane & 7;
-  const int arow0 = (wm * 32 + fr) * 64;
-  const int brow0 = (wn * 32 + fr) * 64;
-
-  gload16(a.ptr(rsA0, 0) + csw, lA0);
-  gload16(a.ptr(rsA1, 0) + csw, lA1);
-  gload16(bsrc.ptr(rsB0, 0) + csw, lB0);
-  gload16(bsrc.ptr(rsB1, 0) + csw, lB1);
-
-  for (int kk = 0; kk < nch; ++kk) {
-    const int cur = kk & 1;
-    if (kk + 1 < nch) {
-      const int nxt = cur ^ 1;
-      gload16(a.ptr(rsA0, kk + 1) + csw, lA0 + nxt * 4096);
-      gload16(a.ptr(rsA1, kk + 1) + csw, lA1 + nxt * 4096);
-      gload16(bsrc.ptr(rsB0, kk + 1) + csw, lB0 + nxt * 4096);
-      gload16(bsrc.ptr(rsB1, kk + 1) + csw, lB1 + nxt * 4096);
-      asm volatile("s_waitcnt vmcnt(4)" ::: "memory");
-    } else {
-      asm volatile("s_waitcnt vmcnt(0)" ::: "memory");
-    }
-    __builtin_amdgcn_s_barrier();
-    __builtin_amdgcn_sched_barrier(0);
-    short8 af[2][2], bf[2][2];
-#pragma unroll
-    for (int fm = 0; fm < 2; ++fm)
-#pragma unroll
-      for (int kh = 0; kh < 2; ++kh) {
-        int slot = ((((kh << 2) | fs) ^ fx) << 3);
-        af[fm][kh] = *(const short8*)(&As[cur][arow0 + fm * 1024 + slot]);
-      }
-#pragma unroll
-    for (int fn = 0; fn < 2; ++fn)
-#pragma unroll
-      for (int kh = 0; kh < 2; ++kh) {
-        int slot = ((((kh << 2) | fs) ^ fx) << 3);
-        bf[fn][kh] = *(const short8*)(&Bs[cur][brow0 + fn * 1024 + slot]);
-      }
-#pragma unroll
-    for (int kh = 0; kh < 2; ++kh)
-#pragma unroll
-      for (int fm = 0; fm < 2; ++fm)
-#pragma unroll
-        for (int fn = 0; fn < 2; ++fn)
-          acc[fm][fn] = __builtin_amdgcn_mfma_f32_16x16x32_bf16(af[fm][kh], bf[fn][kh], acc[fm][fn], 0, 0, 0);
-    __builtin_amdgcn_sched_barrier(0);
-    __builtin_amdgcn_s_barrier();
-  }
-
-  const long ip = p0 + wm * 32 + fs * 4;
-  const int jb = j0 + wn * 32 + fr;
-#pragma unroll
-  for (int fm = 0; fm < 2; ++fm)
-#pragma unroll
-    for (int fn = 0; fn < 2; ++fn)
-#pragma unroll
-      for (int rr = 0; rr < 4; ++rr)
-        epi(ip + fm * 16 + rr, jb + fn * 16, acc[fm][fn][rr]);
-}
-
-
-template <class AS, class BS, class EPI>
-__global__ __launch_bounds__(256, 3) void gemm128(AS a, BS bsrc, int gy, int gp, int nchw, EPI epi) {
-  __shared__ u16 As[8192];
-  __shared__ u16 Bs[8192];
-  const int N = gridDim.x;
-  const int q = N >> 3, r8 = N & 7;
-  const int j8 = blockIdx.x & 7, pos = blockIdx.x >> 3;
-  const int lid = (j8 < r8) ? j8 * (q + 1) + pos : r8 * (q + 1) + (j8 - r8) * q + pos;
-  const int gyp = gy * gp;
-  const int bx = lid / gyp;
-  const int rem = lid - bx * gyp;
-  const int by = rem % gy;
-  const int part = rem / gy;
-  const int k0 = part * nchw;
-
-  const int tid = threadIdx.x;
-  const int w = tid >> 6, lane = tid & 63;
-  const int wm = w >> 1, wn = w & 1;
-  const long p0 = (long)by * 128;
-  const int j0 = bx * 128;
-
-  const int r0 = tid >> 3;
-  const int csw = (((lane & 7) ^ (lane >> 3)) << 3);
-  typename AS::RS rsA[4];
-  typename BS::RS rsB[4];
-#pragma unroll
-  for (int i = 0; i < 4; ++i) {
-    rsA[i] = a.row(p0 + r0 + 32 * i);
-    rsB[i] = bsrc.row(by, (long)j0 + r0 + 32 * i);
-  }
-
-  f32x4 acc[4][4];
-#pragma unroll
-  for (int x = 0; x < 4; ++x)
-#pragma unroll
-    for (int y = 0; y < 4; ++y) acc[x][y] = (f32x4){0.f, 0.f, 0.f, 0.f};
-
-  const int fr = lane & 15, fs = lane >> 4, fx = lane & 7;
-
-  for (int kk = 0; kk < nchw; ++kk) {
-    __syncthreads();
-#pragma unroll
-    for (int i = 0; i < 4; ++i) {
-      gload16(a.ptr(rsA[i], k0 + kk) + csw, As + (i * 32 + w * 8) * 64);
-      gload16(bsrc.ptr(rsB[i], k0 + kk) + csw, Bs + (i * 32 + w * 8) * 64);
-    }
-    __syncthreads();
-#pragma unroll
-    for (int kh = 0; kh < 2; ++kh) {
-      const int slot = ((((kh << 2) | fs) ^ fx) << 3);
-      short8 af[4], bf[4];
-#pragma unroll
-      for (int i = 0; i < 4; ++i) {
-        af[i] = *(const short8*)(As + (wm * 64 + i * 16 + fr) * 64 + slot);
-        bf[i] = *(const short8*)(Bs + (wn * 64 + i * 16 + fr) * 64 + slot);
-      }
-#pragma unroll
-      for (int fm = 0; fm < 4; ++fm)
-#pragma unroll
-        for (int fn = 0; fn < 4; ++fn)
-          acc[fm][fn] = __builtin_amdgcn_mfma_f32_16x16x32_bf16(af[fm], bf[fn], acc[fm][fn], 0, 0, 0);
-    }
-  }
-
-  const long ip = p0 + wm * 64 + fs * 4;
-  const int jb = j0 + wn * 64 + fr;
-#pragma unroll
-  for (int fm = 0; fm < 4; ++fm)
-#pragma unroll
-    for (int fn = 0; fn < 4; ++fn)
-#pragma unroll
-      for (int rr = 0; rr < 4; ++rr)
-        epi(part, ip + fm * 16 + rr, jb + fn * 16, acc[fm][fn][rr]);
-}
-
-template <class EPI>
-__global__ void k_sum_parts(const float* __restrict__ buf, long pstride, int np,
-                            int jw, int jvalid, EPI epi) {
-  long p = blockIdx.x;
-  const float* src = buf + p * (long)jw;
-  for (int j = threadIdx.x; j < jvalid; j += 256) {
-    float v = 0.f;
-    for (int t = 0; t < np; ++t) v += src[t * pstride + j];
-    epi(p, j, v);
-  }
-}
-
-__global__ void k_sum_sgsb(const float* __restrict__ buf, long pstride,
-                           const float* __restrict__ bsg, const float* __restrict__ bsb,
-                           const float* __restrict__ xa, const float* __restrict__ st,
-                           float* __restrict__ xl) {
-  __shared__ float sgb[640];
-  __shared__ float ms[32], rss[32];
-  long p = blockIdx.x;
-  int b = (int)(p / 81), pp = (int)(p - (long)b * 81);
-  const float* src = buf + p * 640;
-  for (int j = threadIdx.x; j < 640; j += 256) {
-    float v = 0.f;
-#pragma unroll
-    for (int t = 0; t < 4; ++t) v += src[t * pstride + j];
-    sgb[j] = v + (j < 320 ? bsg[j] : bsb[j - 320]);
-  }
-  if (threadIdx.x < 32) {
-    ms[threadIdx.x] = st[(b * 32 + threadIdx.x) * 2];
-    rss[threadIdx.x] = st[(b * 32 + threadIdx.x) * 2 + 1];
-  }
-  __syncthreads();
-  for (int c = threadIdx.x; c < 320; c += 256) {
-    int g = c / 10;
-    float xv = xa[((long)b * 128 + pp) * 320 + c];
-    xl[((long)b * 81 + pp) * 320 + c] = (xv - ms[g]) * rss[g] * sgb[c] + sgb[320 + c];
-  }
-}
-
-
 extern "C" void kernel_launch(void* const* d_in, const int* in_sizes, int n_in,
                               void* d_out, int out_size, void* d_ws, size_t ws_size,
                               hipStream_t stream) {
@@ -693,7 +736,7 @@
   u16* Wq2     = (u16*)(base + 109748224);
   u16* Wv_r    = (u16*)(base + 110239744);
   u16* Wsgsb   = (u16*)(base + 117317632);
-  float* partK = (float*)(base + 129114112);
+  float* partV = (float*)(base + 129114112);
   float* xa_f  = (float*)(base + 154279936);
   u16* zpage   = Wv_r + (size_t)320 * 9216;
 
@@ -706,26 +749,17 @@
 
   k_prep0<<<4096, 256, 0, stream>>>(ctx, cond, gx, bbox, Wk, Wq, Wv, Wsg, Wsb,
                                     cmean, cnst, roix, Wk2, Wq2, Wv_r, Wsgsb);
-  k_ctx_prep<<<dim3(4, 16, 32), 256, 0, stream>>>(ctx, cmean, cnst, cn_g, cn_b, cond, sel, bvc, cn2);
-  k_stats810<<<1024, 256, 0, stream>>>(roix, lnst, 1e-6f);
+  k_prep1<<<3072, 256, 0, stream>>>(ctx, cmean, cnst, cn_g, cn_b, cond, sel, bvc, cn2,
+                                    roix, lnst);
   k_aq2<<<6144, 256, 0, stream>>>(roix, lnst, ln_g, ln_b, ind, Aq2);
 
-  gemm128<<<384, 256, 0, stream>>>(TriA{cn2, 2048, 16}, TriB{Wk2, 2048, 16, 0},
-                                   64, 2, 24, EpiPart{partK, (long)8192 * 384, 384});
-  k_sum_parts<<<8192, 256, 0, stream>>>(partK, (long)8192 * 384, 2, 384, 320, EpiHiLo{k2, bk});
-  gemm_pipe<<<320, 256, 0, stream>>>(TriA{Aq2, 768, 6}, TriB{Wq2, 768, 6, 0},
-                                     64, 18, EpiHiLo{q2, bq});
-  gemm128<<<576, 256, 0, stream>>>(ShiftVA{sel, zpage}, ShiftWB{Wv_r},
-                                   64, 3, 48, EpiPart{part_f, (long)8192 * 384, 384});
-  k_sumv_t<<<dim3(4, 5, 32), 256, 0, stream>>>(part_f, (long)8192 * 384, bv, bvc);
-  gemm_pipe<<<256, 256, 0, stream>>>(TriA{q2, 640, 5}, TriB{k2, 640, 5, 256},
-                                     64, 15, EpiLog{attn_out});
+  k_gemms<<<896, 256, 0, stream>>>(cn2, Wk2, k2, bk, sel, Wv_r, zpage, partV,
+                                   Aq2, Wq2, q2, bq);
+  k_mid<<<896, 256, 0, stream>>>(partV, bv, bvc, q2, k2, attn_out);
   k_softmax2<<<dim3(128, 32), 256, 0, stream>>>(attn_out, attn_bf);
   gemm_pipe<<<1344, 256, 0, stream>>>(RowA{attn_bf, 256}, RowB{bvc, 256, 1344},
                                       64, 4, EpiXaAc{xa_f, ac_bf});
-  k_stats_xa<<<1024, 256, 0, stream>>>(xa_f, xast);
-  gemm128<<<420, 256, 0, stream>>>(Shift9A{ac_bf, zpage}, ShiftWB{Wsgsb},
-                                   21, 4, 36, EpiPart{part_f, (long)2688 * 640, 640});
+  k_post<<<1444, 256, 0, stream>>>(xa_f, xast, ac_bf, zpage, Wsgsb, part_f);
   k_sum_sgsb<<<2592, 256, 0, stream>>>(part_f, (long)2688 * 640, bsg, bsb, xa_f, xast, xloc);
 
   k_paste<<<10240, 256, 0, stream>>>(gx, bbox, xloc, out);
```

Result: faster. 318.3 us (-9.3%).
